# Performance work log

Hardware: AMD Instinct MI355X
Metric: run time of the kernel (lower is better)

Reference implementation:

```python
import jax, jax.numpy as jnp
import numpy as np


def setup_inputs() -> dict:
    key = jax.random.key(0)
    k1, k2 = jax.random.split(key)
    B, T, D = 8, 2048, 2048
    layer_in = jax.random.normal(k1, (B, T, D), dtype=jnp.float32)
    # nn.Linear(2D, 2D): weight [out=2D, in=2D], bias [2D]
    W_gate = jax.random.normal(k2, (2 * D, 2 * D), dtype=jnp.float32) * 0.02
    b_gate = jnp.zeros((2 * D,), dtype=jnp.float32)
    return {"layer_in": layer_in, "W_gate": W_gate, "b_gate": b_gate}


def reference(layer_in, W_gate, b_gate):
    # Cumulative average: tril(ones)/row_index @ x  ==  cumsum(x)/[1..t]
    t = layer_in.shape[1]
    denom = jnp.arange(1, t + 1, dtype=layer_in.dtype)[:, None]  # (t, 1)
    average_out = jnp.cumsum(layer_in, axis=1) / denom  # (B, t, D)
    # Gating: Linear(2D -> 2D) on concat(x, avg), then chunk into two gates
    gating_in = jnp.concatenate([layer_in, average_out], axis=-1)  # (B, t, 2D)
    gates = jnp.einsum('btk,ok->bto', gating_in, W_gate) + b_gate  # (B, t, 2D)
    input_gate, forget_gate = jnp.split(gates, 2, axis=2)
    gating_out = (jax.nn.sigmoid(input_gate) * layer_in
                  + jax.nn.sigmoid(forget_gate) * average_out)
    return gating_out, average_out
```

## Files before the change

### kernel.cpp

```cpp
#include <hip/hip_runtime.h>
#include <hip/hip_bf16.h>


#define Bb 8
#define Tt 2048
#define Dd 2048
#define Mm (Bb * Tt)
#define Kk 4096
#define NC 32
#define CT 64

typedef __bf16 bf16x8 __attribute__((ext_vector_type(8)));
typedef float f32x4 __attribute__((ext_vector_type(4)));

__device__ __forceinline__ void gload16(const void* g, void* l) {
    __builtin_amdgcn_global_load_lds(
        (const __attribute__((address_space(1))) unsigned int*)g,
        (__attribute__((address_space(3))) unsigned int*)l, 16, 0, 0);
}

__global__ void wconv_kernel(const float* __restrict__ W,
                             unsigned short* __restrict__ Wb, long n) {
    long i = ((long)blockIdx.x * blockDim.x + threadIdx.x) * 4;
    long stride = (long)gridDim.x * blockDim.x * 4;
    for (; i < n; i += stride) {
        float4 v = *(const float4*)(W + i);
        __hip_bfloat16 a = __float2bfloat16(v.x);
        __hip_bfloat16 b = __float2bfloat16(v.y);
        __hip_bfloat16 c = __float2bfloat16(v.z);
        __hip_bfloat16 d = __float2bfloat16(v.w);
        ushort4 u;
        u.x = *(unsigned short*)&a; u.y = *(unsigned short*)&b;
        u.z = *(unsigned short*)&c; u.w = *(unsigned short*)&d;
        *(ushort4*)(Wb + i) = u;
    }
}

__global__ void ksum_kernel(const float* __restrict__ X, float* __restrict__ S) {
    int d = blockIdx.y * 256 + threadIdx.x;
    int bc = blockIdx.x;
    int b = bc >> 5, c = bc & 31;
    const float* p = X + ((long)(b * Tt + c * CT)) * Dd + d;
    float s = 0.f;
#pragma unroll 8
    for (int t = 0; t < CT; ++t) s += p[(long)t * Dd];
    S[(long)bc * Dd + d] = s;
}

__global__ void kscan_kernel(const float* __restrict__ X, const float* __restrict__ S,
                             float* __restrict__ AVG, unsigned short* __restrict__ Gin) {
    int d = blockIdx.y * 256 + threadIdx.x;
    int bc = blockIdx.x;
    int b = bc >> 5, c = bc & 31;
    const float* Sp = S + (long)(b * NC) * Dd + d;
    float run = 0.f;
    for (int cc = 0; cc < c; ++cc) run += Sp[(long)cc * Dd];
    const float* p = X + ((long)(b * Tt + c * CT)) * Dd + d;
    long row = (long)b * Tt + c * CT;
    for (int tt = 0; tt < CT; ++tt) {
        float x = p[(long)tt * Dd];
        run += x;
        float av = run / (float)(c * CT + tt + 1);
        long r = row + tt;
        AVG[r * Dd + d] = av;
        __hip_bfloat16 xb = __float2bfloat16(x);
        __hip_bfloat16 ab = __float2bfloat16(av);
        Gin[r * 4096 + d] = *(unsigned short*)&xb;
        Gin[r * 4096 + 2048 + d] = *(unsigned short*)&ab;
    }
}

#define MFMA(va, vb, c_) c_ = __builtin_amdgcn_mfma_f32_16x16x32_bf16(va, vb, c_, 0, 0, 0)
#define RD(p_, i_) (*(const bf16x8*)((p_) + (i_) * 1024))
#define SBAR __builtin_amdgcn_s_barrier()
#define SCHB __builtin_amdgcn_sched_barrier(0)
#define LGKM0 do { asm volatile("s_waitcnt lgkmcnt(0)" ::: "memory"); SCHB; } while (0)

#define CL_LO(B0_, B1_, B2_, B3_)                                               \
    __builtin_amdgcn_s_setprio(1);                                              \
    MFMA(aL0,B0_,acc[0][0]); MFMA(aL0,B1_,acc[0][1]); MFMA(aL0,B2_,acc[0][2]); MFMA(aL0,B3_,acc[0][3]); \
    MFMA(aL1,B0_,acc[1][0]); MFMA(aL1,B1_,acc[1][1]); MFMA(aL1,B2_,acc[1][2]); MFMA(aL1,B3_,acc[1][3]); \
    MFMA(aL2,B0_,acc[2][0]); MFMA(aL2,B1_,acc[2][1]); MFMA(aL2,B2_,acc[2][2]); MFMA(aL2,B3_,acc[2][3]); \
    MFMA(aL3,B0_,acc[3][0]); MFMA(aL3,B1_,acc[3][1]); MFMA(aL3,B2_,acc[3][2]); MFMA(aL3,B3_,acc[3][3]); \
    __builtin_amdgcn_s_setprio(0);
#define CL_HI(B0_, B1_, B2_, B3_)                                               \
    __builtin_amdgcn_s_setprio(1);                                              \
    MFMA(aH0,B0_,acc[4][0]); MFMA(aH0,B1_,acc[4][1]); MFMA(aH0,B2_,acc[4][2]); MFMA(aH0,B3_,acc[4][3]); \
    MFMA(aH1,B0_,acc[5][0]); MFMA(aH1,B1_,acc[5][1]); MFMA(aH1,B2_,acc[5][2]); MFMA(aH1,B3_,acc[5][3]); \
    MFMA(aH2,B0_,acc[6][0]); MFMA(aH2,B1_,acc[6][1]); MFMA(aH2,B2_,acc[6][2]); MFMA(aH2,B3_,acc[6][3]); \
    MFMA(aH3,B0_,acc[7][0]); MFMA(aH3,B1_,acc[7][1]); MFMA(aH3,B2_,acc[7][2]); MFMA(aH3,B3_,acc[7][3]); \
    __builtin_amdgcn_s_setprio(0);

#define TILE64(t_, bb_, STG_, RDX_, VM_, VB_)                                   \
  {                                                                             \
    const char* pa_ = rA0 + (bb_);                                              \
    const char* pb_ = rB0 + (bb_);                                              \
    const char* qa_ = rA0 + ((bb_) ^ 65536);                                    \
    const char* qb_ = rB0 + ((bb_) ^ 65536);                                    \
    char* nb_ = ldsb + ((bb_) ^ 65536) + woff;                                  \
    const long ko_ = ((long)(t_) + 1) * 128;                                    \
         \
    LGKM0;                                                         \
                     \
    aH0 = RD(pa_,4); aH1 = RD(pa_,5); aH2 = RD(pa_,6); aH3 = RD(pa_,7);         \
    if (STG_) { gload16(gA0 + ko_, nb_); gload16(gA1 + ko_, nb_ + 8192); }      \
    SCHB;                                                                       \
    CL_LO(bb0, bb1, bb2, bb3)                                                   \
    SCHB;                                                                       \
    asm volatile("s_waitcnt vmcnt(" #VM_ ")" ::: "memory");                     \
    SBAR; SCHB;                                             \
    LGKM0;                                                         \
             \
    aL0 = RD(pa_+32768,0); aL1 = RD(pa_+32768,1); aL2 = RD(pa_+32768,2); aL3 = RD(pa_+32768,3); \
    bd0 = RD(pb_+32768,0); bd1 = RD(pb_+32768,1); bd2 = RD(pb_+32768,2); bd3 = RD(pb_+32768,3); \
    if (STG_) { gload16(gB0 + ko_, nb_ + 16384); gload16(gB1 + ko_, nb_ + 24576); } \
    SCHB;                                                                       \
    CL_HI(bb0, bb1, bb2, bb3)                                                   \
    SCHB;                                                                       \
    LGKM0;                                                         \
           \
    aH0 = RD(pa_+32768,4); aH1 = RD(pa_+32768,5); aH2 = RD(pa_+32768,6); aH3 = RD(pa_+32768,7); \
    if (STG_) { gload16(gA0 + ko_ + 64, nb_ + 32768); gload16(gA1 + ko_ + 64, nb_ + 40960); \
                gload16(gB0 + ko_ + 64, nb_ + 49152); gload16(gB1 + ko_ + 64, nb_ + 57344); } \
    SCHB;                                                                       \
    CL_LO(bd0, bd1, bd2, bd3)                                                   \
    SCHB;                                                                       \
    asm volatile("s_waitcnt vmcnt(" #VB_ ")" ::: "memory");                     \
    SBAR; SCHB;                                           \
    LGKM0;                                                         \
                 \
    if (RDX_) {                                                                 \
      aL0 = RD(qa_,0); aL1 = RD(qa_,1); aL2 = RD(qa_,2); aL3 = RD(qa_,3);       \
      bb0 = RD(qb_,0); bb1 = RD(qb_,1); bb2 = RD(qb_,2); bb3 = RD(qb_,3);       \
    }                                                                           \
    SCHB;                                                                       \
    CL_HI(bd0, bd1, bd2, bd3)                                                   \
    SCHB;                                                                       \
  }

__global__ __launch_bounds__(512) void gemmfh_kernel(
    const unsigned short* __restrict__ Gin,
    const unsigned short* __restrict__ Wb,
    const float* __restrict__ bias,
    float* __restrict__ OUT)
{
    __shared__ __attribute__((aligned(128))) char lds[131072];
    char* ldsb = (char*)lds;

    const int tid = threadIdx.x;
    const int w = tid >> 6, l = tid & 63;
    const int wm = w >> 2, wn = w & 3;
    const int lm = l & 15;
    const int woff = w * 1024;

    const int bid = blockIdx.x;
    const int batch = bid >> 8;
    const int rr = bid & 255;
    const int xcd = rr & 7;
    const int j = rr >> 3;
    const int nt = xcd * 2 + (j >> 4);
    const int mt = batch * 16 + (j & 15);
    const long m0 = (long)mt * 256;
    const int n0 = nt * 128;

    const int srow = tid >> 2;
    const int schunk = (tid & 3) ^ ((tid >> 3) & 3);
    const char* gA0 = (const char*)Gin + (m0 + srow) * 8192 + schunk * 16;
    const char* gA1 = gA0 + 128 * 8192;
    const long jr0 = n0 + ((srow >> 6) << 5) + (srow & 31) + (((srow >> 5) & 1) << 11);
    const int j1 = 128 + srow;
    const long jr1 = n0 + ((j1 >> 6) << 5) + (j1 & 31) + (((j1 >> 5) & 1) << 11);
    const char* gB0 = (const char*)Wb + jr0 * 8192 + schunk * 16;
    const char* gB1 = (const char*)Wb + jr1 * 8192 + schunk * 16;

    const int cbyte = (((l >> 4) ^ ((lm >> 1) & 3))) * 16;
    const char* rA0 = ldsb + (wm * 128 + lm) * 64 + cbyte;
    const char* rB0 = ldsb + 16384 + (wn * 64 + lm) * 64 + cbyte;

    f32x4 acc[8][4] = {};

    bf16x8 aL0, aL1, aL2, aL3, aH0, aH1, aH2, aH3;
    bf16x8 bb0, bb1, bb2, bb3, bd0, bd1, bd2, bd3;

    gload16(gA0,      ldsb + woff);
    gload16(gA1,      ldsb + 8192 + woff);
    gload16(gB0,      ldsb + 16384 + woff);
    gload16(gB1,      ldsb + 24576 + woff);
    gload16(gA0 + 64, ldsb + 32768 + woff);
    gload16(gA1 + 64, ldsb + 40960 + woff);
    gload16(gB0 + 64, ldsb + 49152 + woff);
    gload16(gB1 + 64, ldsb + 57344 + woff);
    asm volatile("s_waitcnt vmcnt(4)" ::: "memory");
    SBAR; SCHB;
    aL0 = RD(rA0,0); aL1 = RD(rA0,1); aL2 = RD(rA0,2); aL3 = RD(rA0,3);
    bb0 = RD(rB0,0); bb1 = RD(rB0,1); bb2 = RD(rB0,2); bb3 = RD(rB0,3);
    SCHB;

#pragma unroll 1
    for (int t = 0; t < 62; t += 2) {
        TILE64(t,     0,     1, 1, 2, 4)
        TILE64(t + 1, 65536, 1, 1, 2, 4)
    }
    TILE64(62, 0,     1, 1, 2, 4)
    TILE64(63, 65536, 0, 0, 0, 0)

#pragma unroll
    for (int mi = 0; mi < 8; ++mi) {
        long rbase = m0 + wm * 128 + mi * 16 + (l >> 4) * 4;
#pragma unroll
        for (int nj = 0; nj < 2; ++nj) {
            int d = n0 + wn * 32 + nj * 16 + lm;
            float bi_ = bias[d];
            float bf_ = bias[d + 2048];
#pragma unroll
            for (int r = 0; r < 4; ++r) {
                long row = rbase + r;
                unsigned int ux = Gin[row * 4096 + d];
                unsigned int ua = Gin[row * 4096 + 2048 + d];
                union { unsigned int u; float f; } cx, ca;
                cx.u = ux << 16; ca.u = ua << 16;
                float gi = acc[mi][nj][r] + bi_;
                float gf = acc[mi][nj + 2][r] + bf_;
                float si = 1.f / (1.f + __expf(-gi));
                float sf = 1.f / (1.f + __expf(-gf));
                OUT[row * 2048 + d] = si * cx.f + sf * ca.f;
            }
        }
    }
}

extern "C" void kernel_launch(void* const* d_in, const int* in_sizes, int n_in,
                              void* d_out, int out_size, void* d_ws, size_t ws_size,
                              hipStream_t stream) {
    const float* X = (const float*)d_in[0];
    const float* W = (const float*)d_in[1];
    const float* bias = (const float*)d_in[2];

    float* OUT = (float*)d_out;
    float* AVG = OUT + (long)Mm * Dd;

    char* ws = (char*)d_ws;
    unsigned short* Wb  = (unsigned short*)ws;
    unsigned short* Gin = (unsigned short*)(ws + 33554432);
    float* S = (float*)(ws + 33554432 + 134217728);

    wconv_kernel<<<2048, 256, 0, stream>>>(W, Wb, (long)Kk * Kk);
    ksum_kernel<<<dim3(Bb * NC, Dd / 256), 256, 0, stream>>>(X, S);
    kscan_kernel<<<dim3(Bb * NC, Dd / 256), 256, 0, stream>>>(X, S, AVG, Gin);
    gemmfh_kernel<<<1024, 512, 0, stream>>>(Gin, Wb, bias, OUT);
}
```

Before: 624.1 us.

## Replace full LDS waits with partial lgkmcnt waits and double-buffered fragment registers

```diff
diff --git a/kernel.cpp b/kernel.cpp
--- a/kernel.cpp
+++ b/kernel.cpp
@@ -74,24 +74,24 @@
 #define RD(p_, i_) (*(const bf16x8*)((p_) + (i_) * 1024))
 #define SBAR __builtin_amdgcn_s_barrier()
 #define SCHB __builtin_amdgcn_sched_barrier(0)
-#define LGKM0 do { asm volatile("s_waitcnt lgkmcnt(0)" ::: "memory"); SCHB; } while (0)
-
-#define CL_LO(B0_, B1_, B2_, B3_)                                               \
+#define LGKMC(N_) do { asm volatile("s_waitcnt lgkmcnt(" #N_ ")" ::: "memory"); SCHB; } while (0)
+
+#define CLUSTER_LO(A0_,A1_,A2_,A3_,B0_,B1_,B2_,B3_)                             \
     __builtin_amdgcn_s_setprio(1);                                              \
-    MFMA(aL0,B0_,acc[0][0]); MFMA(aL0,B1_,acc[0][1]); MFMA(aL0,B2_,acc[0][2]); MFMA(aL0,B3_,acc[0][3]); \
-    MFMA(aL1,B0_,acc[1][0]); MFMA(aL1,B1_,acc[1][1]); MFMA(aL1,B2_,acc[1][2]); MFMA(aL1,B3_,acc[1][3]); \
-    MFMA(aL2,B0_,acc[2][0]); MFMA(aL2,B1_,acc[2][1]); MFMA(aL2,B2_,acc[2][2]); MFMA(aL2,B3_,acc[2][3]); \
-    MFMA(aL3,B0_,acc[3][0]); MFMA(aL3,B1_,acc[3][1]); MFMA(aL3,B2_,acc[3][2]); MFMA(aL3,B3_,acc[3][3]); \
+    MFMA(A0_,B0_,acc[0][0]); MFMA(A0_,B1_,acc[0][1]); MFMA(A0_,B2_,acc[0][2]); MFMA(A0_,B3_,acc[0][3]); \
+    MFMA(A1_,B0_,acc[1][0]); MFMA(A1_,B1_,acc[1][1]); MFMA(A1_,B2_,acc[1][2]); MFMA(A1_,B3_,acc[1][3]); \
+    MFMA(A2_,B0_,acc[2][0]); MFMA(A2_,B1_,acc[2][1]); MFMA(A2_,B2_,acc[2][2]); MFMA(A2_,B3_,acc[2][3]); \
+    MFMA(A3_,B0_,acc[3][0]); MFMA(A3_,B1_,acc[3][1]); MFMA(A3_,B2_,acc[3][2]); MFMA(A3_,B3_,acc[3][3]); \
     __builtin_amdgcn_s_setprio(0);
-#define CL_HI(B0_, B1_, B2_, B3_)                                               \
+#define CLUSTER_HI(A0_,A1_,A2_,A3_,B0_,B1_,B2_,B3_)                             \
     __builtin_amdgcn_s_setprio(1);                                              \
-    MFMA(aH0,B0_,acc[4][0]); MFMA(aH0,B1_,acc[4][1]); MFMA(aH0,B2_,acc[4][2]); MFMA(aH0,B3_,acc[4][3]); \
-    MFMA(aH1,B0_,acc[5][0]); MFMA(aH1,B1_,acc[5][1]); MFMA(aH1,B2_,acc[5][2]); MFMA(aH1,B3_,acc[5][3]); \
-    MFMA(aH2,B0_,acc[6][0]); MFMA(aH2,B1_,acc[6][1]); MFMA(aH2,B2_,acc[6][2]); MFMA(aH2,B3_,acc[6][3]); \
-    MFMA(aH3,B0_,acc[7][0]); MFMA(aH3,B1_,acc[7][1]); MFMA(aH3,B2_,acc[7][2]); MFMA(aH3,B3_,acc[7][3]); \
+    MFMA(A0_,B0_,acc[4][0]); MFMA(A0_,B1_,acc[4][1]); MFMA(A0_,B2_,acc[4][2]); MFMA(A0_,B3_,acc[4][3]); \
+    MFMA(A1_,B0_,acc[5][0]); MFMA(A1_,B1_,acc[5][1]); MFMA(A1_,B2_,acc[5][2]); MFMA(A1_,B3_,acc[5][3]); \
+    MFMA(A2_,B0_,acc[6][0]); MFMA(A2_,B1_,acc[6][1]); MFMA(A2_,B2_,acc[6][2]); MFMA(A2_,B3_,acc[6][3]); \
+    MFMA(A3_,B0_,acc[7][0]); MFMA(A3_,B1_,acc[7][1]); MFMA(A3_,B2_,acc[7][2]); MFMA(A3_,B3_,acc[7][3]); \
     __builtin_amdgcn_s_setprio(0);
 
-#define TILE64(t_, bb_, STG_, RDX_, VM_, VB_)                                   \
+#define TILE64(t_, bb_, STG_, RDX_, VMs_, VBs_, WM3_)                           \
   {                                                                             \
     const char* pa_ = rA0 + (bb_);                                              \
     const char* pb_ = rB0 + (bb_);                                              \
@@ -99,46 +99,44 @@
     const char* qb_ = rB0 + ((bb_) ^ 65536);                                    \
     char* nb_ = ldsb + ((bb_) ^ 65536) + woff;                                  \
     const long ko_ = ((long)(t_) + 1) * 128;                                    \
-         \
-    LGKM0;                                                         \
-                     \
-    aH0 = RD(pa_,4); aH1 = RD(pa_,5); aH2 = RD(pa_,6); aH3 = RD(pa_,7);         \
+                                       \
+    LGKMC(4);                                       \
     if (STG_) { gload16(gA0 + ko_, nb_); gload16(gA1 + ko_, nb_ + 8192); }      \
     SCHB;                                                                       \
-    CL_LO(bb0, bb1, bb2, bb3)                                                   \
-    SCHB;                                                                       \
-    asm volatile("s_waitcnt vmcnt(" #VM_ ")" ::: "memory");                     \
+    CLUSTER_LO(aL0,aL1,aL2,aL3,bb0,bb1,bb2,bb3)                 \
+    SCHB;                                                                       \
+    asm volatile("s_waitcnt vmcnt(" #VMs_ ")" ::: "memory");                    \
     SBAR; SCHB;                                             \
-    LGKM0;                                                         \
-             \
-    aL0 = RD(pa_+32768,0); aL1 = RD(pa_+32768,1); aL2 = RD(pa_+32768,2); aL3 = RD(pa_+32768,3); \
+    cL0 = RD(pa_+32768,0); cL1 = RD(pa_+32768,1); cL2 = RD(pa_+32768,2); cL3 = RD(pa_+32768,3); \
     bd0 = RD(pb_+32768,0); bd1 = RD(pb_+32768,1); bd2 = RD(pb_+32768,2); bd3 = RD(pb_+32768,3); \
+    SCHB;                                                                       \
+    LGKMC(8);                                       \
     if (STG_) { gload16(gB0 + ko_, nb_ + 16384); gload16(gB1 + ko_, nb_ + 24576); } \
     SCHB;                                                                       \
-    CL_HI(bb0, bb1, bb2, bb3)                                                   \
-    SCHB;                                                                       \
-    LGKM0;                                                         \
-           \
-    aH0 = RD(pa_+32768,4); aH1 = RD(pa_+32768,5); aH2 = RD(pa_+32768,6); aH3 = RD(pa_+32768,7); \
+    CLUSTER_HI(aH0,aH1,aH2,aH3,bb0,bb1,bb2,bb3)                 \
+    SCHB;                                                                       \
+    cH0 = RD(pa_+32768,4); cH1 = RD(pa_+32768,5); cH2 = RD(pa_+32768,6); cH3 = RD(pa_+32768,7); \
+    SCHB;                                                                       \
+    LGKMC(4);                                       \
     if (STG_) { gload16(gA0 + ko_ + 64, nb_ + 32768); gload16(gA1 + ko_ + 64, nb_ + 40960); \
                 gload16(gB0 + ko_ + 64, nb_ + 49152); gload16(gB1 + ko_ + 64, nb_ + 57344); } \
     SCHB;                                                                       \
-    CL_LO(bd0, bd1, bd2, bd3)                                                   \
-    SCHB;                                                                       \
-    asm volatile("s_waitcnt vmcnt(" #VB_ ")" ::: "memory");                     \
+    CLUSTER_LO(cL0,cL1,cL2,cL3,bd0,bd1,bd2,bd3)                 \
+    SCHB;                                                                       \
+    asm volatile("s_waitcnt vmcnt(" #VBs_ ")" ::: "memory");                    \
     SBAR; SCHB;                                           \
-    LGKM0;                                                         \
-                 \
     if (RDX_) {                                                                 \
       aL0 = RD(qa_,0); aL1 = RD(qa_,1); aL2 = RD(qa_,2); aL3 = RD(qa_,3);       \
       bb0 = RD(qb_,0); bb1 = RD(qb_,1); bb2 = RD(qb_,2); bb3 = RD(qb_,3);       \
+      aH0 = RD(qa_,4); aH1 = RD(qa_,5); aH2 = RD(qa_,6); aH3 = RD(qa_,7);       \
     }                                                                           \
     SCHB;                                                                       \
-    CL_HI(bd0, bd1, bd2, bd3)                                                   \
+    LGKMC(WM3_);                               \
+    CLUSTER_HI(cH0,cH1,cH2,cH3,bd0,bd1,bd2,bd3)                 \
     SCHB;                                                                       \
   }
 
-__global__ __launch_bounds__(512) void gemmfh_kernel(
+__global__ __launch_bounds__(512) void gemmcl_kernel(
     const unsigned short* __restrict__ Gin,
     const unsigned short* __restrict__ Wb,
     const float* __restrict__ bias,
@@ -180,7 +178,9 @@
     f32x4 acc[8][4] = {};
 
     bf16x8 aL0, aL1, aL2, aL3, aH0, aH1, aH2, aH3;
-    bf16x8 bb0, bb1, bb2, bb3, bd0, bd1, bd2, bd3;
+    bf16x8 bb0, bb1, bb2, bb3;
+    bf16x8 cL0, cL1, cL2, cL3, cH0, cH1, cH2, cH3;
+    bf16x8 bd0, bd1, bd2, bd3;
 
     gload16(gA0,      ldsb + woff);
     gload16(gA1,      ldsb + 8192 + woff);
@@ -194,15 +194,16 @@
     SBAR; SCHB;
     aL0 = RD(rA0,0); aL1 = RD(rA0,1); aL2 = RD(rA0,2); aL3 = RD(rA0,3);
     bb0 = RD(rB0,0); bb1 = RD(rB0,1); bb2 = RD(rB0,2); bb3 = RD(rB0,3);
+    aH0 = RD(rA0,4); aH1 = RD(rA0,5); aH2 = RD(rA0,6); aH3 = RD(rA0,7);
     SCHB;
 
 #pragma unroll 1
     for (int t = 0; t < 62; t += 2) {
-        TILE64(t,     0,     1, 1, 2, 4)
-        TILE64(t + 1, 65536, 1, 1, 2, 4)
-    }
-    TILE64(62, 0,     1, 1, 2, 4)
-    TILE64(63, 65536, 0, 0, 0, 0)
+        TILE64(t,     0,     1, 1, 2, 4, 12)
+        TILE64(t + 1, 65536, 1, 1, 2, 4, 12)
+    }
+    TILE64(62, 0,     1, 1, 2, 4, 12)
+    TILE64(63, 65536, 0, 0, 0, 0, 0)
 
 #pragma unroll
     for (int mi = 0; mi < 8; ++mi) {
@@ -247,5 +248,5 @@
     wconv_kernel<<<2048, 256, 0, stream>>>(W, Wb, (long)Kk * Kk);
     ksum_kernel<<<dim3(Bb * NC, Dd / 256), 256, 0, stream>>>(X, S);
     kscan_kernel<<<dim3(Bb * NC, Dd / 256), 256, 0, stream>>>(X, S, AVG, Gin);
-    gemmfh_kernel<<<1024, 512, 0, stream>>>(Gin, Wb, bias, OUT);
-}
+    gemmcl_kernel<<<1024, 512, 0, stream>>>(Gin, Wb, bias, OUT);
+}
```

Measured after the change: 658.5 us. +5.5%, slower.
